# Performance work log

Measured on AMD Instinct MI355X. Metric: run time of the kernel, lower is better.

## Reference

```python
import jax, jax.numpy as jnp
import numpy as np

N_NODES = 50000


def _gcn_layer(x, W, b, src, dst, n_nodes):
    # GCNConv: h = D^{-1/2} (A + I) D^{-1/2} (x W) + b, with src/dst already
    # including self-loops.
    h = x @ W  # [N, out]
    deg = jax.ops.segment_sum(jnp.ones(src.shape, x.dtype), dst,
                              num_segments=n_nodes)  # [N]
    dinv = jnp.where(deg > 0, jax.lax.rsqrt(jnp.maximum(deg, 1e-12)), 0.0)
    norm = dinv[src] * dinv[dst]  # [E+N]
    msg = h[src] * norm[:, None]  # gathered + weighted messages
    out = jax.ops.segment_sum(msg, dst, num_segments=n_nodes)  # scatter-add
    return out + b


def setup_inputs() -> dict:
    key = jax.random.key(0)
    k0, k1, k2, k3 = jax.random.split(key, 4)
    d_in, hidden, n_edges = 128, 128, 800000
    x = jax.random.normal(k0, (N_NODES, d_in), dtype=jnp.float32)
    edge_index = jax.random.randint(k1, (2, n_edges), 0, N_NODES, dtype=jnp.int64)
    W1 = jax.random.normal(k2, (d_in, hidden), dtype=jnp.float32) * (1.0 / np.sqrt(d_in))
    b1 = jnp.zeros((hidden,), jnp.float32)
    W2 = jax.random.normal(k3, (hidden, hidden), dtype=jnp.float32) * (1.0 / np.sqrt(hidden))
    b2 = jnp.zeros((hidden,), jnp.float32)
    return {"x": x, "edge_index": edge_index, "W1": W1, "b1": b1,
            "W2": W2, "b2": b2}


def reference(x, edge_index, W1, b1, W2, b2):
    n = x.shape[0]
    loop = jnp.arange(n, dtype=edge_index.dtype)
    src = jnp.concatenate([edge_index[0], loop])  # add self-loops
    dst = jnp.concatenate([edge_index[1], loop])
    h = _gcn_layer(x, W1, b1, src, dst, n)
    h = jax.nn.relu(h)
    # dropout p=0.5 is identity in eval mode (self.training == False)
    h = _gcn_layer(h, W2, b2, src, dst, n)
    return jax.nn.log_softmax(h, axis=1)
```

## Files before the change

kernel.cpp:

```cpp
#include <hip/hip_runtime.h>
#include <math.h>

#define D 128
#define CAP 6144
#define EPB 4096
#define SENT 0xFFFFFFFFu

typedef __attribute__((ext_vector_type(8))) short bf16x8;
typedef __attribute__((ext_vector_type(4))) float f32x4;

__device__ __forceinline__ float bf_lo(unsigned u) { return __uint_as_float(u << 16); }
__device__ __forceinline__ float bf_hi(unsigned u) { return __uint_as_float(u & 0xFFFF0000u); }
__device__ __forceinline__ unsigned pack_bf16(float a, float b) {
    unsigned ua = __float_as_uint(a), ub = __float_as_uint(b);
    ua = (ua + 0x7FFFu + ((ua >> 16) & 1u)) >> 16;
    ub = (ub + 0x7FFFu + ((ub >> 16) & 1u)) >> 16;
    return ua | (ub << 16);
}

__device__ __forceinline__ int edge_at(const void* eidx, int i64, long long pos) {
    return i64 ? (int)((const long long*)eidx)[pos] : ((const int*)eidx)[pos];
}


template <int AF32>
__device__ __forceinline__ void gemm_body(char* lds, int bid, const void* Ain,
                                          const float* __restrict__ Wf,
                                          unsigned* __restrict__ yout, int n) {
    int tid = threadIdx.x;
    #pragma unroll
    for (int it = 0; it < 32; ++it) {
        int idx = tid + it * 256;
        int c = idx & 127, k2 = idx >> 7;
        *(unsigned*)&lds[c * 272 + k2 * 4] =
            pack_bf16(Wf[(k2 * 2) * D + c], Wf[(k2 * 2 + 1) * D + c]);
    }
    int w = tid >> 6, l = tid & 63;
    int row0 = bid * 128;
    int rowA0 = row0 + w * 16 + (l & 15);
    int rowA1 = rowA0 + 64;
    int rA0 = rowA0 < n ? rowA0 : 0;
    int rA1 = rowA1 < n ? rowA1 : 0;
    __syncthreads();

    f32x4 acc[2][8];
    #pragma unroll
    for (int r = 0; r < 2; ++r)
        #pragma unroll
        for (int f = 0; f < 8; ++f) acc[r][f] = (f32x4)0.f;

    #pragma unroll
    for (int s = 0; s < 4; ++s) {
        bf16x8 a0, a1;
        if (AF32) {
            const float* Af = (const float*)Ain;
            const float4* p0 = (const float4*)(Af + (size_t)rA0 * D + ((l >> 4) << 3) + s * 32);
            const float4* p1 = (const float4*)(Af + (size_t)rA1 * D + ((l >> 4) << 3) + s * 32);
            float4 f0 = p0[0], f1 = p0[1], f2 = p1[0], f3 = p1[1];
            uint4 v0, v1;
            v0.x = pack_bf16(f0.x, f0.y); v0.y = pack_bf16(f0.z, f0.w);
            v0.z = pack_bf16(f1.x, f1.y); v0.w = pack_bf16(f1.z, f1.w);
            v1.x = pack_bf16(f2.x, f2.y); v1.y = pack_bf16(f2.z, f2.w);
            v1.z = pack_bf16(f3.x, f3.y); v1.w = pack_bf16(f3.z, f3.w);
            a0 = *(bf16x8*)&v0;
            a1 = *(bf16x8*)&v1;
        } else {
            const char* Ab = (const char*)Ain;
            a0 = *(const bf16x8*)(Ab + (size_t)rA0 * 256 + ((l >> 4) << 4) + s * 64);
            a1 = *(const bf16x8*)(Ab + (size_t)rA1 * 256 + ((l >> 4) << 4) + s * 64);
        }
        int boff = ((l >> 4) << 4) + s * 64;
        #pragma unroll
        for (int f = 0; f < 8; ++f) {
            bf16x8 b = *(const bf16x8*)&lds[(f * 16 + (l & 15)) * 272 + boff];
            acc[0][f] = __builtin_amdgcn_mfma_f32_16x16x32_bf16(a0, b, acc[0][f], 0, 0, 0);
            acc[1][f] = __builtin_amdgcn_mfma_f32_16x16x32_bf16(a1, b, acc[1][f], 0, 0, 0);
        }
    }

    float* fl = (float*)lds;
    #pragma unroll
    for (int r = 0; r < 2; ++r) {
        __syncthreads();
        {
            int rbase = w * 16 + ((l >> 4) << 2);
            #pragma unroll
            for (int f = 0; f < 8; ++f) {
                int c = f * 16 + (l & 15);
                #pragma unroll
                for (int j = 0; j < 4; ++j)
                    fl[(rbase + j) * 132 + c] = acc[r][f][j];
            }
        }
        __syncthreads();
        int row = tid >> 2, cseg = (tid & 3) << 5;
        int gr = row0 + r * 64 + row;
        if (gr < n) {
            uint4* ob = (uint4*)yout + (size_t)gr * 16 + ((tid & 3) << 2);
            #pragma unroll
            for (int q = 0; q < 4; ++q) {
                uint4 v;
                v.x = pack_bf16(fl[row * 132 + cseg + q * 8 + 0], fl[row * 132 + cseg + q * 8 + 1]);
                v.y = pack_bf16(fl[row * 132 + cseg + q * 8 + 2], fl[row * 132 + cseg + q * 8 + 3]);
                v.z = pack_bf16(fl[row * 132 + cseg + q * 8 + 4], fl[row * 132 + cseg + q * 8 + 5]);
                v.w = pack_bf16(fl[row * 132 + cseg + q * 8 + 6], fl[row * 132 + cseg + q * 8 + 7]);
                ob[q] = v;
            }
        }
    }
}


__global__ void __launch_bounds__(256) k_prep(const void* eidx, int* bcnt,
                                              unsigned* __restrict__ binned, int e,
                                              const float* __restrict__ x,
                                              const float* __restrict__ W1,
                                              unsigned* __restrict__ y1,
                                              int n, int ebk) {
    __shared__ char lds[35840];
    int b = blockIdx.x, t = threadIdx.x;

    if (b >= ebk) {
        gemm_body<1>(lds, b - ebk, x, W1, y1, n);
        return;
    }

    int* hist = (int*)lds;
    int* gbase = hist + 256;
    int* lcur = gbase + 256;
    uint2* ed = (uint2*)(lds + 3072);

    const int* e32 = (const int*)eidx;
    int i64 = 1;
    #pragma unroll
    for (int j = 1; j < 32; j += 2)
        if (e32[j] != 0) i64 = 0;

    hist[t] = 0;
    lcur[t] = 0;
    __syncthreads();
    long long base = (long long)b * EPB;
    #pragma unroll
    for (int k = 0; k < EPB / 256; ++k) {
        long long i = base + k * 256 + t;
        if (i < e) {
            int s = edge_at(eidx, i64, i);
            int d = edge_at(eidx, i64, (long long)e + i);
            ed[k * 256 + t] = make_uint2((unsigned)s, (unsigned)d);
            atomicAdd(&hist[d >> 8], 1);
        }
    }
    __syncthreads();
    int c = hist[t];
    int cpad = (c + 15) & ~15;
    gbase[t] = cpad ? atomicAdd(&bcnt[t], cpad) : 0;
    __syncthreads();
    long long rem = e - base;
    int lim = (rem < EPB) ? (int)rem : EPB;
    for (int j = t; j < lim; j += 256) {
        uint2 sd = ed[j];
        int bk = sd.y >> 8;
        int off = gbase[bk] + atomicAdd(&lcur[bk], 1);
        if (off >= CAP) off = CAP - 1;
        binned[(size_t)bk * CAP + off] = sd.x | ((sd.y & 255u) << 17);
    }
    __syncthreads();
    int gb_ = gbase[t];
    for (int j = c; j < cpad; ++j)
        binned[(size_t)t * CAP + gb_ + j] = SENT;
}


__global__ void __launch_bounds__(256) k_binB(const unsigned* __restrict__ binned,
                                              const int* __restrict__ bcnt,
                                              unsigned* __restrict__ meta,
                                              unsigned* __restrict__ csr64,
                                              unsigned* __restrict__ y1,
                                              int n) {
    __shared__ int lcur[256];
    int b = blockIdx.x, t = threadIdx.x;
    if (b == 0) {
        if (t < 64) y1[(size_t)n * 64 + t] = 0;
        if (t == 64) meta[n] = 0;
    }
    lcur[t] = 0;
    __syncthreads();

    int cnt = bcnt[b];
    if (cnt > CAP) cnt = CAP;
    unsigned nodebase = (unsigned)b << 8;
    for (int i = t; i < cnt; i += 256) {
        unsigned en = binned[(size_t)b * CAP + i];
        if (en == SENT) continue;
        unsigned src = en & 0x1FFFF;
        unsigned dl = en >> 17;
        int pos = atomicAdd(&lcur[dl], 1);
        if (pos < 64)
            csr64[(size_t)(nodebase + dl) * 64 + pos] = src;
    }
    __syncthreads();

    int node = b * 256 + t;
    if (node < n) {
        int dv = lcur[t];
        int filled = dv < 64 ? dv : 64;
        int pend = (filled + 15) & ~15;
        for (int j = filled; j < pend; ++j)
            csr64[(size_t)node * 64 + j] = (unsigned)n;
        unsigned q = __float2uint_rn(rsqrtf((float)(dv + 1)) * 32767.0f);
        meta[node] = (q << 17) | (unsigned)(pend >> 4);
    }
}


template <int EPI>
__global__ void __launch_bounds__(256) k_agg(const unsigned* __restrict__ Y,
                                             const unsigned* __restrict__ meta,
                                             const unsigned* __restrict__ csr64,
                                             const float* __restrict__ bias,
                                             void* __restrict__ outp, int n) {
    int node = __builtin_amdgcn_readfirstlane(blockIdx.x * 4 + (threadIdx.x >> 6));
    if (node >= n) return;
    int lane = threadIdx.x & 63;
    unsigned mt = meta[node];
    unsigned us = Y[(size_t)node * 64 + lane];
    const unsigned* cp = csr64 + (size_t)node * 64;

    int gcnt = mt & 7;
    float di = (float)(mt >> 17) * (1.0f / 32767.0f);
    float ax = 0.f, ay = 0.f;

    for (int g = 0; g < gcnt; ++g) {
        #pragma unroll
        for (int k2 = 0; k2 < 16; ++k2) {
            unsigned s_ = cp[g * 16 + k2];
            float q = (float)(meta[s_] >> 17);
            unsigned u = Y[(size_t)s_ * 64 + lane];
            ax += q * bf_lo(u);
            ay += q * bf_hi(u);
        }
    }

    float2 bv = ((const float2*)bias)[lane];
    float z0 = di * (ax * (1.0f / 32767.0f) + di * bf_lo(us)) + bv.x;
    float z1 = di * (ay * (1.0f / 32767.0f) + di * bf_hi(us)) + bv.y;

    if (EPI == 0) {
        ((unsigned*)outp)[(size_t)node * 64 + lane] =
            pack_bf16(fmaxf(z0, 0.f), fmaxf(z1, 0.f));
    } else {
        float m = fmaxf(z0, z1);
        #pragma unroll
        for (int off = 1; off < 64; off <<= 1) m = fmaxf(m, __shfl_xor(m, off));
        float s = __expf(z0 - m) + __expf(z1 - m);
        #pragma unroll
        for (int off = 1; off < 64; off <<= 1) s += __shfl_xor(s, off);
        float lse = m + __logf(s);
        ((float2*)outp)[(size_t)node * 64 + lane] = make_float2(z0 - lse, z1 - lse);
    }
}


__global__ void __launch_bounds__(256) k_gemm2(const unsigned* __restrict__ h,
                                               const float* __restrict__ W2,
                                               unsigned* __restrict__ y2, int n) {
    __shared__ char lds[34816];
    gemm_body<0>(lds, blockIdx.x, h, W2, y2, n);
}


extern "C" void kernel_launch(void* const* d_in, const int* in_sizes, int n_in,
                              void* d_out, int out_size, void* d_ws, size_t ws_size,
                              hipStream_t stream) {
    const float* x  = (const float*)d_in[0];
    const void* eix = d_in[1];
    const float* W1 = (const float*)d_in[2];
    const float* b1 = (const float*)d_in[3];
    const float* W2 = (const float*)d_in[4];
    const float* b2 = (const float*)d_in[5];
    float* out = (float*)d_out;
    int n = in_sizes[0] / D;
    int e = in_sizes[1] / 2;

    char* p = (char*)d_ws;
    auto carve = [&](size_t bytes) -> void* {
        void* r = (void*)p;
        p += (bytes + 255) & ~(size_t)255;
        return r;
    };
    unsigned* meta   = (unsigned*)carve((size_t)(n + 1) * 4);
    int*      bcnt   = (int*)carve(1024);
    unsigned* csr64  = (unsigned*)carve((size_t)n * 64 * 4);
    unsigned* binned = (unsigned*)carve((size_t)256 * CAP * 4);
    unsigned* y1     = (unsigned*)carve((size_t)(n + 1) * 64 * 4);
    unsigned* h      = (unsigned*)carve((size_t)n * 64 * 4);

    int nb = (n + 255) / 256;
    int ebk = (e + EPB - 1) / EPB;
    int gb = (n + 127) / 128;
    int ab = (n + 3) / 4;

    hipMemsetAsync(bcnt, 0, 1024, stream);
    k_prep<<<ebk + gb, 256, 0, stream>>>(eix, bcnt, binned, e, x, W1, y1, n, ebk);
    k_binB<<<nb, 256, 0, stream>>>(binned, bcnt, meta, csr64, y1, n);
    k_agg<0><<<ab, 256, 0, stream>>>(y1, meta, csr64, b1, h, n);
    k_gemm2<<<gb, 256, 0, stream>>>(h, W2, y1, n);
    k_agg<1><<<ab, 256, 0, stream>>>(y1, meta, csr64, b2, out, n);
}
```

Baseline: 145.1 us.

## Quantize layer-1 features to int8 with per-row scales and pad neighbor lists to 4

The first-layer GEMM now emits int8 features with a per-row scale instead of bf16. The scale is folded with the degree normalization into a per-node factor, so the first aggregation gathers half the bytes per neighbor. Neighbor lists are padded to multiples of 4 instead of 16, which removes the sentinel padding in the binning stage and cuts wasted gathers. Both aggregation kernels are unrolled by 4. Int8 quantization adds rounding error that may push accuracy close to tolerance.

```diff
diff --git a/kernel.cpp b/kernel.cpp
--- a/kernel.cpp
+++ b/kernel.cpp
@@ -4,7 +4,6 @@
 #define D 128
 #define CAP 6144
 #define EPB 4096
-#define SENT 0xFFFFFFFFu
 
 typedef __attribute__((ext_vector_type(8))) short bf16x8;
 typedef __attribute__((ext_vector_type(4))) float f32x4;
@@ -23,10 +22,12 @@
 }
 
 
-template <int AF32>
+template <int AF32, int OUT8>
 __device__ __forceinline__ void gemm_body(char* lds, int bid, const void* Ain,
                                           const float* __restrict__ Wf,
-                                          unsigned* __restrict__ yout, int n) {
+                                          unsigned* __restrict__ ybf,
+                                          unsigned char* __restrict__ y8,
+                                          float* __restrict__ scales, int n) {
     int tid = threadIdx.x;
     #pragma unroll
     for (int it = 0; it < 32; ++it) {
@@ -96,15 +97,40 @@
         int row = tid >> 2, cseg = (tid & 3) << 5;
         int gr = row0 + r * 64 + row;
         if (gr < n) {
-            uint4* ob = (uint4*)yout + (size_t)gr * 16 + ((tid & 3) << 2);
+            float z[32];
             #pragma unroll
-            for (int q = 0; q < 4; ++q) {
-                uint4 v;
-                v.x = pack_bf16(fl[row * 132 + cseg + q * 8 + 0], fl[row * 132 + cseg + q * 8 + 1]);
-                v.y = pack_bf16(fl[row * 132 + cseg + q * 8 + 2], fl[row * 132 + cseg + q * 8 + 3]);
-                v.z = pack_bf16(fl[row * 132 + cseg + q * 8 + 4], fl[row * 132 + cseg + q * 8 + 5]);
-                v.w = pack_bf16(fl[row * 132 + cseg + q * 8 + 6], fl[row * 132 + cseg + q * 8 + 7]);
-                ob[q] = v;
+            for (int i = 0; i < 32; ++i) z[i] = fl[row * 132 + cseg + i];
+            if (OUT8) {
+                float mx = 0.f;
+                #pragma unroll
+                for (int i = 0; i < 32; ++i) mx = fmaxf(mx, fabsf(z[i]));
+                mx = fmaxf(mx, __shfl_xor(mx, 1));
+                mx = fmaxf(mx, __shfl_xor(mx, 2));
+                float inv = mx > 0.f ? 127.0f / mx : 0.f;
+                unsigned q[8];
+                #pragma unroll
+                for (int j = 0; j < 8; ++j) {
+                    int q0 = __float2int_rn(z[j * 4 + 0] * inv);
+                    int q1 = __float2int_rn(z[j * 4 + 1] * inv);
+                    int q2 = __float2int_rn(z[j * 4 + 2] * inv);
+                    int q3 = __float2int_rn(z[j * 4 + 3] * inv);
+                    q[j] = (q0 & 255) | ((q1 & 255) << 8) | ((q2 & 255) << 16) | ((q3 & 255) << 24);
+                }
+                uint4* op = (uint4*)(y8 + (size_t)gr * 128 + cseg);
+                op[0] = make_uint4(q[0], q[1], q[2], q[3]);
+                op[1] = make_uint4(q[4], q[5], q[6], q[7]);
+                if ((tid & 3) == 0) scales[gr] = mx * (1.0f / 127.0f);
+            } else {
+                uint4* ob = (uint4*)ybf + (size_t)gr * 16 + ((tid & 3) << 2);
+                #pragma unroll
+                for (int qd = 0; qd < 4; ++qd) {
+                    uint4 v;
+                    v.x = pack_bf16(z[qd * 8 + 0], z[qd * 8 + 1]);
+                    v.y = pack_bf16(z[qd * 8 + 2], z[qd * 8 + 3]);
+                    v.z = pack_bf16(z[qd * 8 + 4], z[qd * 8 + 5]);
+                    v.w = pack_bf16(z[qd * 8 + 6], z[qd * 8 + 7]);
+                    ob[qd] = v;
+                }
             }
         }
     }
@@ -115,13 +141,14 @@
                                               unsigned* __restrict__ binned, int e,
                                               const float* __restrict__ x,
                                               const float* __restrict__ W1,
-                                              unsigned* __restrict__ y1,
+                                              unsigned char* __restrict__ y8,
+                                              float* __restrict__ scales,
                                               int n, int ebk) {
     __shared__ char lds[35840];
     int b = blockIdx.x, t = threadIdx.x;
 
     if (b >= ebk) {
-        gemm_body<1>(lds, b - ebk, x, W1, y1, n);
+        gemm_body<1, 1>(lds, b - ebk, x, W1, nullptr, y8, scales, n);
         return;
     }
 
@@ -152,8 +179,7 @@
     }
     __syncthreads();
     int c = hist[t];
-    int cpad = (c + 15) & ~15;
-    gbase[t] = cpad ? atomicAdd(&bcnt[t], cpad) : 0;
+    gbase[t] = c ? atomicAdd(&bcnt[t], c) : 0;
     __syncthreads();
     long long rem = e - base;
     int lim = (rem < EPB) ? (int)rem : EPB;
@@ -164,24 +190,23 @@
         if (off >= CAP) off = CAP - 1;
         binned[(size_t)bk * CAP + off] = sd.x | ((sd.y & 255u) << 17);
     }
-    __syncthreads();
-    int gb_ = gbase[t];
-    for (int j = c; j < cpad; ++j)
-        binned[(size_t)t * CAP + gb_ + j] = SENT;
 }
 
 
 __global__ void __launch_bounds__(256) k_binB(const unsigned* __restrict__ binned,
                                               const int* __restrict__ bcnt,
+                                              const float* __restrict__ scales,
                                               unsigned* __restrict__ meta,
+                                              float* __restrict__ fs,
                                               unsigned* __restrict__ csr64,
-                                              unsigned* __restrict__ y1,
+                                              unsigned* __restrict__ ybf,
                                               int n) {
     __shared__ int lcur[256];
     int b = blockIdx.x, t = threadIdx.x;
     if (b == 0) {
-        if (t < 64) y1[(size_t)n * 64 + t] = 0;
+        if (t < 64) ybf[(size_t)n * 64 + t] = 0;
         if (t == 64) meta[n] = 0;
+        if (t == 65) fs[n] = 0.f;
     }
     lcur[t] = 0;
     __syncthreads();
@@ -191,7 +216,6 @@
     unsigned nodebase = (unsigned)b << 8;
     for (int i = t; i < cnt; i += 256) {
         unsigned en = binned[(size_t)b * CAP + i];
-        if (en == SENT) continue;
         unsigned src = en & 0x1FFFF;
         unsigned dl = en >> 17;
         int pos = atomicAdd(&lcur[dl], 1);
@@ -204,68 +228,103 @@
     if (node < n) {
         int dv = lcur[t];
         int filled = dv < 64 ? dv : 64;
-        int pend = (filled + 15) & ~15;
+        int pend = (filled + 3) & ~3;
         for (int j = filled; j < pend; ++j)
             csr64[(size_t)node * 64 + j] = (unsigned)n;
         unsigned q = __float2uint_rn(rsqrtf((float)(dv + 1)) * 32767.0f);
-        meta[node] = (q << 17) | (unsigned)(pend >> 4);
-    }
-}
-
-
-template <int EPI>
-__global__ void __launch_bounds__(256) k_agg(const unsigned* __restrict__ Y,
-                                             const unsigned* __restrict__ meta,
-                                             const unsigned* __restrict__ csr64,
-                                             const float* __restrict__ bias,
-                                             void* __restrict__ outp, int n) {
+        meta[node] = (q << 17) | (unsigned)(pend >> 2);
+        fs[node] = ((float)q * (1.0f / 32767.0f)) * scales[node];
+    }
+}
+
+
+__global__ void __launch_bounds__(256) k_agg8(const unsigned char* __restrict__ Y8,
+                                              const float* __restrict__ fs,
+                                              const unsigned* __restrict__ meta,
+                                              const unsigned* __restrict__ csr64,
+                                              const float* __restrict__ bias,
+                                              unsigned* __restrict__ h, int n) {
     int node = __builtin_amdgcn_readfirstlane(blockIdx.x * 4 + (threadIdx.x >> 6));
     if (node >= n) return;
     int lane = threadIdx.x & 63;
     unsigned mt = meta[node];
+    int pend = (mt & 31) << 2;
+    float di = (float)(mt >> 17) * (1.0f / 32767.0f);
+    const unsigned* cp = csr64 + (size_t)node * 64;
+    const unsigned short* Yu = (const unsigned short*)Y8;
+
+    unsigned su = Yu[(size_t)node * 64 + lane];
+    float fself = fs[node];
+    float ax = fself * (float)(char)(su & 255);
+    float ay = fself * (float)(char)(su >> 8);
+
+    for (int e = 0; e < pend; e += 4) {
+        unsigned s0 = cp[e + 0], s1 = cp[e + 1], s2 = cp[e + 2], s3 = cp[e + 3];
+        float f0 = fs[s0], f1 = fs[s1], f2 = fs[s2], f3 = fs[s3];
+        unsigned u0 = Yu[(size_t)s0 * 64 + lane];
+        unsigned u1 = Yu[(size_t)s1 * 64 + lane];
+        unsigned u2 = Yu[(size_t)s2 * 64 + lane];
+        unsigned u3 = Yu[(size_t)s3 * 64 + lane];
+        ax += f0 * (float)(char)(u0 & 255) + f1 * (float)(char)(u1 & 255)
+            + f2 * (float)(char)(u2 & 255) + f3 * (float)(char)(u3 & 255);
+        ay += f0 * (float)(char)(u0 >> 8) + f1 * (float)(char)(u1 >> 8)
+            + f2 * (float)(char)(u2 >> 8) + f3 * (float)(char)(u3 >> 8);
+    }
+
+    float2 bv = ((const float2*)bias)[lane];
+    float z0 = di * ax + bv.x;
+    float z1 = di * ay + bv.y;
+    h[(size_t)node * 64 + lane] = pack_bf16(fmaxf(z0, 0.f), fmaxf(z1, 0.f));
+}
+
+
+__global__ void __launch_bounds__(256) k_agg2(const unsigned* __restrict__ Y,
+                                              const unsigned* __restrict__ meta,
+                                              const unsigned* __restrict__ csr64,
+                                              const float* __restrict__ bias,
+                                              float* __restrict__ outp, int n) {
+    int node = __builtin_amdgcn_readfirstlane(blockIdx.x * 4 + (threadIdx.x >> 6));
+    if (node >= n) return;
+    int lane = threadIdx.x & 63;
+    unsigned mt = meta[node];
+    int pend = (mt & 31) << 2;
+    float di = (float)(mt >> 17) * (1.0f / 32767.0f);
+    const unsigned* cp = csr64 + (size_t)node * 64;
+
     unsigned us = Y[(size_t)node * 64 + lane];
-    const unsigned* cp = csr64 + (size_t)node * 64;
-
-    int gcnt = mt & 7;
-    float di = (float)(mt >> 17) * (1.0f / 32767.0f);
     float ax = 0.f, ay = 0.f;
-
-    for (int g = 0; g < gcnt; ++g) {
-        #pragma unroll
-        for (int k2 = 0; k2 < 16; ++k2) {
-            unsigned s_ = cp[g * 16 + k2];
-            float q = (float)(meta[s_] >> 17);
-            unsigned u = Y[(size_t)s_ * 64 + lane];
-            ax += q * bf_lo(u);
-            ay += q * bf_hi(u);
-        }
+    for (int e = 0; e < pend; e += 4) {
+        unsigned s0 = cp[e + 0], s1 = cp[e + 1], s2 = cp[e + 2], s3 = cp[e + 3];
+        float q0 = (float)(meta[s0] >> 17), q1 = (float)(meta[s1] >> 17);
+        float q2 = (float)(meta[s2] >> 17), q3 = (float)(meta[s3] >> 17);
+        unsigned u0 = Y[(size_t)s0 * 64 + lane];
+        unsigned u1 = Y[(size_t)s1 * 64 + lane];
+        unsigned u2 = Y[(size_t)s2 * 64 + lane];
+        unsigned u3 = Y[(size_t)s3 * 64 + lane];
+        ax += q0 * bf_lo(u0) + q1 * bf_lo(u1) + q2 * bf_lo(u2) + q3 * bf_lo(u3);
+        ay += q0 * bf_hi(u0) + q1 * bf_hi(u1) + q2 * bf_hi(u2) + q3 * bf_hi(u3);
     }
 
     float2 bv = ((const float2*)bias)[lane];
     float z0 = di * (ax * (1.0f / 32767.0f) + di * bf_lo(us)) + bv.x;
     float z1 = di * (ay * (1.0f / 32767.0f) + di * bf_hi(us)) + bv.y;
 
-    if (EPI == 0) {
-        ((unsigned*)outp)[(size_t)node * 64 + lane] =
-            pack_bf16(fmaxf(z0, 0.f), fmaxf(z1, 0.f));
-    } else {
-        float m = fmaxf(z0, z1);
-        #pragma unroll
-        for (int off = 1; off < 64; off <<= 1) m = fmaxf(m, __shfl_xor(m, off));
-        float s = __expf(z0 - m) + __expf(z1 - m);
-        #pragma unroll
-        for (int off = 1; off < 64; off <<= 1) s += __shfl_xor(s, off);
-        float lse = m + __logf(s);
-        ((float2*)outp)[(size_t)node * 64 + lane] = make_float2(z0 - lse, z1 - lse);
-    }
+    float m = fmaxf(z0, z1);
+    #pragma unroll
+    for (int off = 1; off < 64; off <<= 1) m = fmaxf(m, __shfl_xor(m, off));
+    float s = __expf(z0 - m) + __expf(z1 - m);
+    #pragma unroll
+    for (int off = 1; off < 64; off <<= 1) s += __shfl_xor(s, off);
+    float lse = m + __logf(s);
+    ((float2*)outp)[(size_t)node * 64 + lane] = make_float2(z0 - lse, z1 - lse);
 }
 
 
 __global__ void __launch_bounds__(256) k_gemm2(const unsigned* __restrict__ h,
                                                const float* __restrict__ W2,
-                                               unsigned* __restrict__ y2, int n) {
+                                               unsigned* __restrict__ ybf, int n) {
     __shared__ char lds[34816];
-    gemm_body<0>(lds, blockIdx.x, h, W2, y2, n);
+    gemm_body<0, 0>(lds, blockIdx.x, h, W2, ybf, nullptr, nullptr, n);
 }
 
 
@@ -288,12 +347,15 @@
         p += (bytes + 255) & ~(size_t)255;
         return r;
     };
-    unsigned* meta   = (unsigned*)carve((size_t)(n + 1) * 4);
-    int*      bcnt   = (int*)carve(1024);
-    unsigned* csr64  = (unsigned*)carve((size_t)n * 64 * 4);
-    unsigned* binned = (unsigned*)carve((size_t)256 * CAP * 4);
-    unsigned* y1     = (unsigned*)carve((size_t)(n + 1) * 64 * 4);
-    unsigned* h      = (unsigned*)carve((size_t)n * 64 * 4);
+    unsigned*      meta   = (unsigned*)carve((size_t)(n + 1) * 4);
+    float*         fs     = (float*)carve((size_t)(n + 1) * 4);
+    float*         scales = (float*)carve((size_t)(n + 1) * 4);
+    int*           bcnt   = (int*)carve(1024);
+    unsigned*      csr64  = (unsigned*)carve((size_t)n * 64 * 4);
+    unsigned*      binned = (unsigned*)carve((size_t)256 * CAP * 4);
+    unsigned char* y8     = (unsigned char*)carve((size_t)(n + 1) * 128);
+    unsigned*      ybf    = (unsigned*)carve((size_t)(n + 1) * 64 * 4);
+    unsigned*      h      = (unsigned*)carve((size_t)n * 64 * 4);
 
     int nb = (n + 255) / 256;
     int ebk = (e + EPB - 1) / EPB;
@@ -301,9 +363,9 @@
     int ab = (n + 3) / 4;
 
     hipMemsetAsync(bcnt, 0, 1024, stream);
-    k_prep<<<ebk + gb, 256, 0, stream>>>(eix, bcnt, binned, e, x, W1, y1, n, ebk);
-    k_binB<<<nb, 256, 0, stream>>>(binned, bcnt, meta, csr64, y1, n);
-    k_agg<0><<<ab, 256, 0, stream>>>(y1, meta, csr64, b1, h, n);
-    k_gemm2<<<gb, 256, 0, stream>>>(h, W2, y1, n);
-    k_agg<1><<<ab, 256, 0, stream>>>(y1, meta, csr64, b2, out, n);
-}
+    k_prep<<<ebk + gb, 256, 0, stream>>>(eix, bcnt, binned, e, x, W1, y8, scales, n, ebk);
+    k_binB<<<nb, 256, 0, stream>>>(binned, bcnt, scales, meta, fs, csr64, ybf, n);
+    k_agg8<<<ab, 256, 0, stream>>>(y8, fs, meta, csr64, b1, h, n);
+    k_gemm2<<<gb, 256, 0, stream>>>(h, W2, ybf, n);
+    k_agg2<<<ab, 256, 0, stream>>>(ybf, meta, csr64, b2, out, n);
+}
```

Result: faster. 132.7 us (-8.6%).
